# Performance work log

Measured on AMD Instinct MI355X. Metric: run time of the kernel, lower is better.

## Reference

```python
import jax, jax.numpy as jnp
import numpy as np
from jax import lax


def setup_inputs() -> dict:
    key = jax.random.key(0)
    k1, k2, k3, k4 = jax.random.split(key, 4)
    N, D, B, R, EF = 100000, 256, 64, 32, 32
    storage = jax.random.normal(k1, (N, D), dtype=jnp.float32)
    query = jax.random.normal(k2, (B, D), dtype=jnp.float32)
    graph = jax.random.randint(k3, (N, R), 0, N, dtype=jnp.int32)      # fixed-degree NSW adjacency
    initial = jax.random.randint(k4, (B, EF), 0, N, dtype=jnp.int32)   # random entry points (entry())
    return {"query": query, "storage": storage, "graph": graph,
            "initial": initial, "k": 10, "ef_search": EF}


def reference(query, storage, graph, initial, k, ef_search):
    """Batched greedy best-first NSW search (ef_search fixed expansion steps)."""
    N = storage.shape[0]
    INF = jnp.float32(1e30)

    def sqdist(q, ids):
        diff = storage[ids] - q            # [R, D] gather
        return jnp.sum(diff * diff, axis=-1)

    def search_one(q, init):
        cd = sqdist(q, init)                               # candidate distances [EF]
        visited = jnp.zeros((N,), jnp.bool_).at[init].set(True)
        expanded = jnp.zeros((N,), jnp.bool_)

        def step(state, _):
            cid, cd, visited, expanded = state
            # pick closest unexpanded candidate
            pickd = jnp.where(expanded[cid], INF, cd)
            j = jnp.argmin(pickd)
            u = cid[j]
            expanded = expanded.at[u].set(True)
            # expand neighbors of u
            nbrs = graph[u]                                # [R]
            fresh = ~visited[nbrs]
            nd = jnp.where(fresh, sqdist(q, nbrs), INF)    # skip already-visited
            visited = visited.at[nbrs].set(True)
            # merge candidate pool, keep ef_search best
            all_ids = jnp.concatenate([cid, nbrs])
            all_d = jnp.concatenate([cd, nd])
            negd, idx = lax.top_k(-all_d, ef_search)
            return (all_ids[idx], -negd, visited, expanded), None

        (cid, cd, _, _), _ = lax.scan(step, (init, cd, visited, expanded),
                                      None, length=ef_search)
        negk, idx = lax.top_k(-cd, k)
        return cid[idx], -negk

    topk_ids, topk_dists = jax.vmap(search_one)(query, initial)
    return topk_ids, topk_dists
```

## Files before the change

### kernel.cpp

```cpp
#include <hip/hip_runtime.h>


#define DIMS     256
#define RDEG     32
#define EFPOOL   32
#define KOUT     10
#define NBITW    3125
#define INF_D    1e30f

__global__ __launch_bounds__(512) void nsw_search_kernel(
    const float* __restrict__ query,
    const float* __restrict__ storage,
    const int*   __restrict__ graph,
    const int*   __restrict__ initial,
    float*       __restrict__ out,
    int B)
{
    __shared__ unsigned int visited[NBITW];
    __shared__ unsigned int expanded[NBITW];
    __shared__ float pool_d[EFPOOL];
    __shared__ int   pool_id[EFPOOL];
    __shared__ float cand_d[RDEG];
    __shared__ int   cand_id[RDEG];
    __shared__ int   fresh_f[RDEG];
    __shared__ float all_d[2 * EFPOOL];
    __shared__ int   all_id[2 * EFPOOL];
    __shared__ float np_d[EFPOOL];
    __shared__ int   np_id[EFPOOL];
    __shared__ int   s_u;

    const int tid = threadIdx.x;
    const int b   = blockIdx.x;
    const int g   = tid >> 4;
    const int l   = tid & 15;

    for (int i = tid; i < NBITW; i += 512) { visited[i] = 0u; expanded[i] = 0u; }

    float qv[16];
    {
        const float4* qp4 = reinterpret_cast<const float4*>(query + (size_t)b * DIMS + l * 16);
        #pragma unroll
        for (int j = 0; j < 4; ++j) {
            float4 v = qp4[j];
            qv[4*j+0] = v.x; qv[4*j+1] = v.y; qv[4*j+2] = v.z; qv[4*j+3] = v.w;
        }
    }

    if (tid < EFPOOL) {
        int id = initial[b * EFPOOL + tid];
        cand_id[tid] = id;
        atomicOr(&visited[id >> 5], 1u << (id & 31));
    }
    __syncthreads();

    {
        int id = cand_id[g];
        const float4* sp4 = reinterpret_cast<const float4*>(storage + (size_t)id * DIMS + l * 16);
        float acc = 0.f;
        #pragma unroll
        for (int j = 0; j < 4; ++j) {
            float4 s4 = sp4[j];
            float d0 = s4.x - qv[4*j+0]; acc = fmaf(d0, d0, acc);
            float d1 = s4.y - qv[4*j+1]; acc = fmaf(d1, d1, acc);
            float d2 = s4.z - qv[4*j+2]; acc = fmaf(d2, d2, acc);
            float d3 = s4.w - qv[4*j+3]; acc = fmaf(d3, d3, acc);
        }
        #pragma unroll
        for (int m = 1; m < 16; m <<= 1) acc += __shfl_xor(acc, m, 64);
        if (l == 0) { pool_d[g] = acc; pool_id[g] = id; }
    }
    __syncthreads();

    for (int step = 0; step < EFPOOL; ++step) {
        if (tid < 32) {
            int   id = pool_id[tid];
            bool  ex = (expanded[id >> 5] >> (id & 31)) & 1u;
            float pd = ex ? INF_D : pool_d[tid];
            int   ix = tid;
            #pragma unroll
            for (int m = 16; m >= 1; m >>= 1) {
                float od = __shfl_xor(pd, m, 64);
                int   oi = __shfl_xor(ix, m, 64);
                if (od < pd || (od == pd && oi < ix)) { pd = od; ix = oi; }
            }
            if (tid == 0) {
                int u = pool_id[ix];
                s_u = u;
                expanded[u >> 5] |= (1u << (u & 31));
            }
        }
        __syncthreads();
        const int u = s_u;

        if (tid < RDEG) {
            int nb = graph[(size_t)u * RDEG + tid];
            cand_id[tid] = nb;
            fresh_f[tid] = !((visited[nb >> 5] >> (nb & 31)) & 1u);
        }
        __syncthreads();
        if (tid < RDEG) {
            int nb = cand_id[tid];
            if (fresh_f[tid]) atomicOr(&visited[nb >> 5], 1u << (nb & 31));
        }

        {
            int  f  = fresh_f[g];
            int  id = cand_id[g];
            float acc = 0.f;
            if (f) {
                const float4* sp4 = reinterpret_cast<const float4*>(storage + (size_t)id * DIMS + l * 16);
                #pragma unroll
                for (int j = 0; j < 4; ++j) {
                    float4 s4 = sp4[j];
                    float d0 = s4.x - qv[4*j+0]; acc = fmaf(d0, d0, acc);
                    float d1 = s4.y - qv[4*j+1]; acc = fmaf(d1, d1, acc);
                    float d2 = s4.z - qv[4*j+2]; acc = fmaf(d2, d2, acc);
                    float d3 = s4.w - qv[4*j+3]; acc = fmaf(d3, d3, acc);
                }
            }
            #pragma unroll
            for (int m = 1; m < 16; m <<= 1) acc += __shfl_xor(acc, m, 64);
            if (l == 0) cand_d[g] = f ? acc : INF_D;
        }
        __syncthreads();

        if (tid < 64) {
            if (tid < 32) { all_d[tid] = pool_d[tid]; all_id[tid] = pool_id[tid]; }
            else          { all_d[tid] = cand_d[tid - 32]; all_id[tid] = cand_id[tid - 32]; }
        }
        __syncthreads();
        if (tid < 64) {
            float di = all_d[tid];
            int rank = 0;
            #pragma unroll 8
            for (int j = 0; j < 64; ++j) {
                float dj = all_d[j];
                rank += (dj < di || (dj == di && j < tid)) ? 1 : 0;
            }
            if (rank < 32) { np_d[rank] = di; np_id[rank] = all_id[tid]; }
        }
        __syncthreads();
        if (tid < 32) { pool_d[tid] = np_d[tid]; pool_id[tid] = np_id[tid]; }
        __syncthreads();
    }

    if (tid < KOUT) {
        out[b * KOUT + tid]              = (float)pool_id[tid];
        out[B * KOUT + b * KOUT + tid]   = pool_d[tid];
    }
}

extern "C" void kernel_launch(void* const* d_in, const int* in_sizes, int n_in,
                              void* d_out, int out_size, void* d_ws, size_t ws_size,
                              hipStream_t stream) {
    const float* query   = (const float*)d_in[0];
    const float* storage = (const float*)d_in[1];
    const int*   graph   = (const int*)d_in[2];
    const int*   initial = (const int*)d_in[3];
    float* out = (float*)d_out;

    const int B = in_sizes[0] / DIMS;

    nsw_search_kernel<<<B, 512, 0, stream>>>(query, storage, graph, initial, out, B);
}
```

Before: 271.6 us.

## Restructure NSW search into a single-wavefront kernel with register-resident pool

Replaces the 512-thread block with one 64-lane wavefront per query. The candidate pool lives in registers, the argmin and rank-based merge use lane shuffles, and all __syncthreads barriers are removed. Each neighbor's distance is split across two lanes, each loading 128 floats into registers, which gives more memory-level parallelism per lane. This cuts the per-step barrier and shared-memory round-trip latency, but the large register arrays and far fewer threads per block may expose gather latency and spill registers.

```diff
diff --git a/kernel.cpp b/kernel.cpp
--- a/kernel.cpp
+++ b/kernel.cpp
@@ -1,14 +1,14 @@
 #include <hip/hip_runtime.h>
 
 
-#define DIMS     256
-#define RDEG     32
-#define EFPOOL   32
-#define KOUT     10
-#define NBITW    3125
-#define INF_D    1e30f
+#define DIMS   256
+#define RDEG   32
+#define EFPOOL 32
+#define KOUT   10
+#define NWORDS 3125
+#define INF_D  1e30f
 
-__global__ __launch_bounds__(512) void nsw_search_kernel(
+__global__ __launch_bounds__(64, 1) void nsw_wave_kernel(
     const float* __restrict__ query,
     const float* __restrict__ storage,
     const int*   __restrict__ graph,
@@ -16,137 +16,91 @@
     float*       __restrict__ out,
     int B)
 {
-    __shared__ unsigned int visited[NBITW];
-    __shared__ unsigned int expanded[NBITW];
-    __shared__ float pool_d[EFPOOL];
-    __shared__ int   pool_id[EFPOOL];
-    __shared__ float cand_d[RDEG];
-    __shared__ int   cand_id[RDEG];
-    __shared__ int   fresh_f[RDEG];
-    __shared__ float all_d[2 * EFPOOL];
-    __shared__ int   all_id[2 * EFPOOL];
-    __shared__ float np_d[EFPOOL];
-    __shared__ int   np_id[EFPOOL];
-    __shared__ int   s_u;
+    __shared__ unsigned int visited[NWORDS];
+    __shared__ unsigned int expanded[NWORDS];
+    __shared__ float sc_d[EFPOOL];
+    __shared__ int   sc_id[EFPOOL];
 
-    const int tid = threadIdx.x;
-    const int b   = blockIdx.x;
-    const int g   = tid >> 4;
-    const int l   = tid & 15;
+    const int l    = threadIdx.x;
+    const int b    = blockIdx.x;
+    const int nb   = l & 31;
+    const int half = l >> 5;
 
-    for (int i = tid; i < NBITW; i += 512) { visited[i] = 0u; expanded[i] = 0u; }
+    for (int i = l; i < NWORDS; i += 64) { visited[i] = 0u; expanded[i] = 0u; }
 
-    float qv[16];
+    float4 qv[32];
     {
-        const float4* qp4 = reinterpret_cast<const float4*>(query + (size_t)b * DIMS + l * 16);
+        const float4* qp = reinterpret_cast<const float4*>(query + (size_t)b * DIMS) + half * 32;
         #pragma unroll
-        for (int j = 0; j < 4; ++j) {
-            float4 v = qp4[j];
-            qv[4*j+0] = v.x; qv[4*j+1] = v.y; qv[4*j+2] = v.z; qv[4*j+3] = v.w;
-        }
+        for (int j = 0; j < 32; ++j) qv[j] = qp[j];
     }
 
-    if (tid < EFPOOL) {
-        int id = initial[b * EFPOOL + tid];
-        cand_id[tid] = id;
-        atomicOr(&visited[id >> 5], 1u << (id & 31));
+    auto halfdist = [&](int id) -> float {
+        const float4* sp = reinterpret_cast<const float4*>(storage + (size_t)id * DIMS) + half * 32;
+        float4 r[32];
+        #pragma unroll
+        for (int j = 0; j < 32; ++j) r[j] = sp[j];
+        float a0 = 0.f, a1 = 0.f, a2 = 0.f, a3 = 0.f;
+        #pragma unroll
+        for (int j = 0; j < 32; ++j) {
+            float d0 = r[j].x - qv[j].x; a0 = fmaf(d0, d0, a0);
+            float d1 = r[j].y - qv[j].y; a1 = fmaf(d1, d1, a1);
+            float d2 = r[j].z - qv[j].z; a2 = fmaf(d2, d2, a2);
+            float d3 = r[j].w - qv[j].w; a3 = fmaf(d3, d3, a3);
+        }
+        return (a0 + a1) + (a2 + a3);
+    };
+
+    int pool_id = initial[b * EFPOOL + nb];
+    if (l < 32) atomicOr(&visited[pool_id >> 5], 1u << (pool_id & 31));
+    float pool_d;
+    {
+        float part = halfdist(pool_id);
+        pool_d = part + __shfl_xor(part, 32, 64);
     }
-    __syncthreads();
-
-    {
-        int id = cand_id[g];
-        const float4* sp4 = reinterpret_cast<const float4*>(storage + (size_t)id * DIMS + l * 16);
-        float acc = 0.f;
-        #pragma unroll
-        for (int j = 0; j < 4; ++j) {
-            float4 s4 = sp4[j];
-            float d0 = s4.x - qv[4*j+0]; acc = fmaf(d0, d0, acc);
-            float d1 = s4.y - qv[4*j+1]; acc = fmaf(d1, d1, acc);
-            float d2 = s4.z - qv[4*j+2]; acc = fmaf(d2, d2, acc);
-            float d3 = s4.w - qv[4*j+3]; acc = fmaf(d3, d3, acc);
-        }
-        #pragma unroll
-        for (int m = 1; m < 16; m <<= 1) acc += __shfl_xor(acc, m, 64);
-        if (l == 0) { pool_d[g] = acc; pool_id[g] = id; }
-    }
-    __syncthreads();
 
     for (int step = 0; step < EFPOOL; ++step) {
-        if (tid < 32) {
-            int   id = pool_id[tid];
-            bool  ex = (expanded[id >> 5] >> (id & 31)) & 1u;
-            float pd = ex ? INF_D : pool_d[tid];
-            int   ix = tid;
-            #pragma unroll
-            for (int m = 16; m >= 1; m >>= 1) {
-                float od = __shfl_xor(pd, m, 64);
-                int   oi = __shfl_xor(ix, m, 64);
-                if (od < pd || (od == pd && oi < ix)) { pd = od; ix = oi; }
-            }
-            if (tid == 0) {
-                int u = pool_id[ix];
-                s_u = u;
-                expanded[u >> 5] |= (1u << (u & 31));
-            }
+        unsigned ew = expanded[pool_id >> 5];
+        bool ex = (ew >> (pool_id & 31)) & 1u;
+        float pd = ex ? INF_D : pool_d;
+        int   ix = nb;
+        #pragma unroll
+        for (int m = 16; m >= 1; m >>= 1) {
+            float od = __shfl_xor(pd, m, 64);
+            int   oi = __shfl_xor(ix, m, 64);
+            if (od < pd || (od == pd && oi < ix)) { pd = od; ix = oi; }
         }
-        __syncthreads();
-        const int u = s_u;
+        int jx = __builtin_amdgcn_readfirstlane(ix);
+        int u  = __shfl(pool_id, jx, 64);
+        if (l == 0) atomicOr(&expanded[u >> 5], 1u << (u & 31));
 
-        if (tid < RDEG) {
-            int nb = graph[(size_t)u * RDEG + tid];
-            cand_id[tid] = nb;
-            fresh_f[tid] = !((visited[nb >> 5] >> (nb & 31)) & 1u);
+        int nbid = graph[(size_t)u * RDEG + nb];
+        unsigned vw = visited[nbid >> 5];
+        bool fresh = !((vw >> (nbid & 31)) & 1u);
+        if (l < 32 && fresh) atomicOr(&visited[nbid >> 5], 1u << (nbid & 31));
+
+        float part = fresh ? halfdist(nbid) : 0.f;
+        float nd = part + __shfl_xor(part, 32, 64);
+        if (!fresh) nd = INF_D;
+
+        float ed  = half ? nd   : pool_d;
+        int   eid = half ? nbid : pool_id;
+        unsigned long long key =
+            ((unsigned long long)__float_as_uint(ed) << 6) | (unsigned)l;
+        int rank = 0;
+        #pragma unroll
+        for (int j = 0; j < 64; ++j) {
+            unsigned long long kj = __shfl(key, j, 64);
+            rank += (kj < key) ? 1 : 0;
         }
-        __syncthreads();
-        if (tid < RDEG) {
-            int nb = cand_id[tid];
-            if (fresh_f[tid]) atomicOr(&visited[nb >> 5], 1u << (nb & 31));
-        }
-
-        {
-            int  f  = fresh_f[g];
-            int  id = cand_id[g];
-            float acc = 0.f;
-            if (f) {
-                const float4* sp4 = reinterpret_cast<const float4*>(storage + (size_t)id * DIMS + l * 16);
-                #pragma unroll
-                for (int j = 0; j < 4; ++j) {
-                    float4 s4 = sp4[j];
-                    float d0 = s4.x - qv[4*j+0]; acc = fmaf(d0, d0, acc);
-                    float d1 = s4.y - qv[4*j+1]; acc = fmaf(d1, d1, acc);
-                    float d2 = s4.z - qv[4*j+2]; acc = fmaf(d2, d2, acc);
-                    float d3 = s4.w - qv[4*j+3]; acc = fmaf(d3, d3, acc);
-                }
-            }
-            #pragma unroll
-            for (int m = 1; m < 16; m <<= 1) acc += __shfl_xor(acc, m, 64);
-            if (l == 0) cand_d[g] = f ? acc : INF_D;
-        }
-        __syncthreads();
-
-        if (tid < 64) {
-            if (tid < 32) { all_d[tid] = pool_d[tid]; all_id[tid] = pool_id[tid]; }
-            else          { all_d[tid] = cand_d[tid - 32]; all_id[tid] = cand_id[tid - 32]; }
-        }
-        __syncthreads();
-        if (tid < 64) {
-            float di = all_d[tid];
-            int rank = 0;
-            #pragma unroll 8
-            for (int j = 0; j < 64; ++j) {
-                float dj = all_d[j];
-                rank += (dj < di || (dj == di && j < tid)) ? 1 : 0;
-            }
-            if (rank < 32) { np_d[rank] = di; np_id[rank] = all_id[tid]; }
-        }
-        __syncthreads();
-        if (tid < 32) { pool_d[tid] = np_d[tid]; pool_id[tid] = np_id[tid]; }
-        __syncthreads();
+        if (rank < EFPOOL) { sc_d[rank] = ed; sc_id[rank] = eid; }
+        pool_d  = sc_d[nb];
+        pool_id = sc_id[nb];
     }
 
-    if (tid < KOUT) {
-        out[b * KOUT + tid]              = (float)pool_id[tid];
-        out[B * KOUT + b * KOUT + tid]   = pool_d[tid];
+    if (l < KOUT) {
+        out[b * KOUT + l]            = (float)pool_id;
+        out[B * KOUT + b * KOUT + l] = pool_d;
     }
 }
 
@@ -161,5 +115,5 @@
 
     const int B = in_sizes[0] / DIMS;
 
-    nsw_search_kernel<<<B, 512, 0, stream>>>(query, storage, graph, initial, out, B);
+    nsw_wave_kernel<<<B, 64, 0, stream>>>(query, storage, graph, initial, out, B);
 }
```

After: 281.4 us. +3.6%, slower.
